# Optimization experiments

Hardware: AMD Instinct MI355X
Metric: run time of the kernel (lower is better)

Reference implementation:

```python
import jax, jax.numpy as jnp
import numpy as np
from jax.scipy.linalg import expm

DIM = 2048        # state dimension (init arg `dim`)
M_STEPS = 8192    # kernel length (init arg `timestamp`)
DELTA = 0.01      # ZOH step size (init arg `delta`)
STAB = 1e-3       # stabilizer added to A before inversion (matches torch code)


def setup_inputs() -> dict:
    key = jax.random.key(0)
    k1, k2, k3 = jax.random.split(key, 3)
    # Match the torch init scaling so matrix_exp/inv stay well-conditioned.
    A = jnp.eye(DIM, dtype=jnp.float32) * -0.01 \
        + jax.random.normal(k1, (DIM, DIM), dtype=jnp.float32) * 0.001
    B = jax.random.normal(k2, (DIM, 1), dtype=jnp.float32) * 0.01
    C = jax.random.normal(k3, (1, DIM), dtype=jnp.float32) * 0.01
    return {"A": A, "B": B, "C": C, "M": M_STEPS}


def reference(A, B, C, M):
    dim = A.shape[0]
    I = jnp.eye(dim, dtype=A.dtype)
    # --- ZOH discretization (torch._zoh_discretize) ---
    A_bar = expm(DELTA * A)                         # [dim, dim]
    A_inv = jnp.linalg.inv(A + STAB * I)            # [dim, dim]
    B_bar = A_inv @ (A_bar - I) @ (DELTA * B)       # [dim, 1]

    # --- kernel power iteration (torch._compute_K_bar) ---
    # K[t] = C @ A_bar^t @ B_bar. Since B_bar is a vector, the serial
    # matrix-power loop reduces to M sequential matvecs (same math).
    def step(x, _):
        term = (C @ x)[0, 0]        # scalar K_t
        return A_bar @ x, term      # advance state: A_bar^{t+1} B_bar

    _, terms = jax.lax.scan(step, B_bar, None, length=M)  # [M]
    K_bar = terms[::-1][None, :]    # flip along time, shape [1, M]
    return K_bar
```

## Files before the change

### kernel.cpp

```cpp
#include <hip/hip_runtime.h>
#include <hip/hip_bf16.h>


#define DIMN 2048
#define MSTEPS 8192
#define RSPLIT 91
#define NSTEPS 90
#define NN ((size_t)DIMN * DIMN)
#define NBLK 32
#define ALD 40
#define GJP 65

typedef short short8 __attribute__((ext_vector_type(8)));
typedef float f32x4 __attribute__((ext_vector_type(4)));

__device__ inline void split1(float x, unsigned short& h, unsigned short& l)
{
  __hip_bfloat16 b = __float2bfloat16(x);
  h = *reinterpret_cast<unsigned short*>(&b);
  float r = x - __bfloat162float(b);
  __hip_bfloat16 b2 = __float2bfloat16(r);
  l = *reinterpret_cast<unsigned short*>(&b2);
}

__global__ __launch_bounds__(256)
void k_combine4(float* out,
                const float* i1, float c1, const float* i2, float c2,
                const float* i3, float c3, const float* i4, float c4,
                float dval)
{
  const int total = DIMN * DIMN;
  for (int idx = blockIdx.x * 256 + threadIdx.x; idx < total; idx += gridDim.x * 256) {
    float v = 0.f;
    if (i1) v = fmaf(c1, i1[idx], v);
    if (i2) v = fmaf(c2, i2[idx], v);
    if (i3) v = fmaf(c3, i3[idx], v);
    if (i4) v = fmaf(c4, i4[idx], v);
    if ((idx >> 11) == (idx & 2047)) v += dval;
    out[idx] = v;
  }
}

__global__ __launch_bounds__(256)
void k_fill64(const float* __restrict__ A, double* __restrict__ M)
{
  const int total = DIMN * DIMN;
  for (int idx = blockIdx.x * 256 + threadIdx.x; idx < total; idx += gridDim.x * 256) {
    double v = (double)A[idx];
    if ((idx >> 11) == (idx & 2047)) v += 1e-3;
    M[idx] = v;
  }
}

__global__ __launch_bounds__(256)
void k_split(const float* __restrict__ in, unsigned short* __restrict__ hi,
             unsigned short* __restrict__ lo)
{
  const int i4 = blockIdx.x * 256 + threadIdx.x;
  const float4 v = ((const float4*)in)[i4];
  ushort4 h, l;
  split1(v.x, h.x, l.x); split1(v.y, h.y, l.y);
  split1(v.z, h.z, l.z); split1(v.w, h.w, l.w);
  ((ushort4*)hi)[i4] = h;
  ((ushort4*)lo)[i4] = l;
}

__global__ __launch_bounds__(256)
void k_splitT(const float* __restrict__ in, unsigned short* __restrict__ hi,
              unsigned short* __restrict__ lo)
{
  __shared__ float t[32][33];
  const int bx = blockIdx.x * 32, by = blockIdx.y * 32;
  const int lx = threadIdx.x, ly = threadIdx.y;
  for (int dy = 0; dy < 32; dy += 8)
    t[ly + dy][lx] = in[(size_t)(by + ly + dy) * DIMN + bx + lx];
  __syncthreads();
  for (int dy = 0; dy < 32; dy += 8) {
    const size_t o = (size_t)(bx + ly + dy) * DIMN + by + lx;
    unsigned short h, l;
    split1(t[lx][ly + dy], h, l);
    hi[o] = h; lo[o] = l;
  }
}

__global__ __launch_bounds__(256)
void k_gemm3(const unsigned short* __restrict__ Ahg, const unsigned short* __restrict__ Alg,
             const unsigned short* __restrict__ Bhg, const unsigned short* __restrict__ Blg,
             float* __restrict__ C, float alpha,
             const float* E1, float c1, const float* E2, float c2)
{
  __shared__ unsigned short sAh[128 * ALD];
  __shared__ unsigned short sAl[128 * ALD];
  __shared__ unsigned short sBh[128 * ALD];
  __shared__ unsigned short sBl[128 * ALD];
  const int tid = threadIdx.x;
  const int wid = tid >> 6, lane = tid & 63;
  const int lr = lane & 15, lg = lane >> 4;
  const int wm = wid >> 1, wn = wid & 1;
  const int brow = blockIdx.y * 128, bcol = blockIdx.x * 128;
  const int sr = tid >> 1, sh = (tid & 1) * 16;

  const unsigned short* gAh = Ahg + (size_t)(brow + sr) * DIMN + sh;
  const unsigned short* gAl = Alg + (size_t)(brow + sr) * DIMN + sh;
  const unsigned short* gBh = Bhg + (size_t)(bcol + sr) * DIMN + sh;
  const unsigned short* gBl = Blg + (size_t)(bcol + sr) * DIMN + sh;

  f32x4 acc[4][4];
#pragma unroll
  for (int mf = 0; mf < 4; ++mf)
#pragma unroll
    for (int nf = 0; nf < 4; ++nf) acc[mf][nf] = (f32x4){0.f, 0.f, 0.f, 0.f};

  uint4 pa0 = *(const uint4*)gAh;      uint4 pa1 = *(const uint4*)(gAh + 8);
  uint4 pb0 = *(const uint4*)gAl;      uint4 pb1 = *(const uint4*)(gAl + 8);
  uint4 pc0 = *(const uint4*)gBh;      uint4 pc1 = *(const uint4*)(gBh + 8);
  uint4 pd0 = *(const uint4*)gBl;      uint4 pd1 = *(const uint4*)(gBl + 8);

  const int nk = DIMN / 32;
  for (int kt = 0; kt < nk; ++kt) {
    *(uint4*)&sAh[sr * ALD + sh] = pa0;  *(uint4*)&sAh[sr * ALD + sh + 8] = pa1;
    *(uint4*)&sAl[sr * ALD + sh] = pb0;  *(uint4*)&sAl[sr * ALD + sh + 8] = pb1;
    *(uint4*)&sBh[sr * ALD + sh] = pc0;  *(uint4*)&sBh[sr * ALD + sh + 8] = pc1;
    *(uint4*)&sBl[sr * ALD + sh] = pd0;  *(uint4*)&sBl[sr * ALD + sh + 8] = pd1;
    __syncthreads();
    if (kt + 1 < nk) {
      const int o = (kt + 1) * 32;
      pa0 = *(const uint4*)(gAh + o);  pa1 = *(const uint4*)(gAh + o + 8);
      pb0 = *(const uint4*)(gAl + o);  pb1 = *(const uint4*)(gAl + o + 8);
      pc0 = *(const uint4*)(gBh + o);  pc1 = *(const uint4*)(gBh + o + 8);
      pd0 = *(const uint4*)(gBl + o);  pd1 = *(const uint4*)(gBl + o + 8);
    }
#pragma unroll
    for (int mf = 0; mf < 4; ++mf) {
      const int ar = 64 * wm + 16 * mf + lr;
      const short8 ah = *(const short8*)&sAh[ar * ALD + lg * 8];
      const short8 al = *(const short8*)&sAl[ar * ALD + lg * 8];
#pragma unroll
      for (int nf = 0; nf < 4; ++nf) {
        const int br = 64 * wn + 16 * nf + lr;
        const short8 bh = *(const short8*)&sBh[br * ALD + lg * 8];
        const short8 bl = *(const short8*)&sBl[br * ALD + lg * 8];
        acc[mf][nf] = __builtin_amdgcn_mfma_f32_16x16x32_bf16(ah, bh, acc[mf][nf], 0, 0, 0);
        acc[mf][nf] = __builtin_amdgcn_mfma_f32_16x16x32_bf16(ah, bl, acc[mf][nf], 0, 0, 0);
        acc[mf][nf] = __builtin_amdgcn_mfma_f32_16x16x32_bf16(al, bh, acc[mf][nf], 0, 0, 0);
      }
    }
    __syncthreads();
  }
#pragma unroll
  for (int mf = 0; mf < 4; ++mf) {
#pragma unroll
    for (int nf = 0; nf < 4; ++nf) {
      const int col = bcol + 64 * wn + 16 * nf + lr;
#pragma unroll
      for (int i = 0; i < 4; ++i) {
        const int row = brow + 64 * wm + 16 * mf + 4 * lg + i;
        float v = alpha * acc[mf][nf][i];
        if (E1) v = fmaf(c1, E1[(size_t)row * DIMN + col], v);
        if (E2) v = fmaf(c2, E2[(size_t)row * DIMN + col], v);
        C[(size_t)row * DIMN + col] = v;
      }
    }
  }
}

#define DBM 64
#define DBK 8
__global__ __launch_bounds__(256)
void k_dgemm(const double* __restrict__ A, int lda,
             const double* __restrict__ B, int ldb,
             double* C, int ldc, int K, double alpha,
             const double* E1, int ld1, double c1)
{
  __shared__ double As[DBK][DBM];
  __shared__ double Bs[DBK][DBM];
  const int tid = threadIdx.x;
  const int tx = tid & 15, ty = tid >> 4;
  const int brow = blockIdx.y * DBM, bcol = blockIdx.x * DBM;

  const int arow = tid >> 2, ac0 = (tid & 3) * 2;
  const int brw  = tid >> 5, bc0 = (tid & 31) * 2;

  const double* Aptr = A + (size_t)(brow + arow) * lda + ac0;
  const double* Bptr = B + (size_t)brw * ldb + (bcol + bc0);

  double2 aPre = *(const double2*)Aptr;
  double2 bPre = *(const double2*)Bptr;

  double acc[4][4];
#pragma unroll
  for (int i = 0; i < 4; ++i)
#pragma unroll
    for (int j = 0; j < 4; ++j) acc[i][j] = 0.0;

  const int nk = K / DBK;
  for (int kt = 0; kt < nk; ++kt) {
    As[ac0 + 0][arow] = aPre.x;
    As[ac0 + 1][arow] = aPre.y;
    Bs[brw][bc0 + 0] = bPre.x;
    Bs[brw][bc0 + 1] = bPre.y;
    __syncthreads();
    if (kt + 1 < nk) {
      aPre = *(const double2*)(Aptr + (size_t)(kt + 1) * DBK);
      bPre = *(const double2*)(Bptr + (size_t)(kt + 1) * DBK * ldb);
    }
#pragma unroll
    for (int kk = 0; kk < DBK; ++kk) {
      double a[4], b[4];
#pragma unroll
      for (int i = 0; i < 4; ++i) a[i] = As[kk][ty * 4 + i];
#pragma unroll
      for (int j = 0; j < 4; ++j) b[j] = Bs[kk][tx * 4 + j];
#pragma unroll
      for (int i = 0; i < 4; ++i)
#pragma unroll
        for (int j = 0; j < 4; ++j)
          acc[i][j] = fma(a[i], b[j], acc[i][j]);
    }
    __syncthreads();
  }
#pragma unroll
  for (int i = 0; i < 4; ++i) {
    const int gi = brow + ty * 4 + i;
#pragma unroll
    for (int j = 0; j < 4; ++j) {
      const int gj = bcol + tx * 4 + j;
      double v = alpha * acc[i][j];
      if (E1) v = fma(c1, E1[(size_t)gi * ld1 + gj], v);
      C[(size_t)gi * ldc + gj] = v;
    }
  }
}

__global__ __launch_bounds__(256)
void k_gj64(const double* __restrict__ M, int ldm, double* __restrict__ W, int ldw)
{
  __shared__ double a[128][GJP];
  const int tid = threadIdx.x;
  const int rg = tid & 7;
  const int cg = tid >> 3;

  for (int idx = tid; idx < 64 * 64; idx += 256) {
    const int r = idx >> 6, c = idx & 63;
    a[c][r] = M[(size_t)r * ldm + c];
    a[64 + c][r] = (r == c) ? 1.0 : 0.0;
  }
  __syncthreads();

  for (int p = 0; p < 64; ++p) {
    const double rpv = 1.0 / a[p][p];
    const int c0 = p + 1 + cg;
    const int c1 = c0 + 32;
    const double prs0 = a[c0][p] * rpv;
    const double prs1 = a[c1][p] * rpv;
    double colp[8];
#pragma unroll
    for (int k = 0; k < 4; ++k) {
      const double2 t2 = *(const double2*)&a[p][rg * 8 + 2 * k];
      colp[2 * k] = t2.x; colp[2 * k + 1] = t2.y;
    }
    __syncthreads();
#pragma unroll
    for (int k = 0; k < 8; ++k) {
      const int r = rg * 8 + k;
      const bool isp = (r == p);
      const double v0 = a[c0][r];
      const double v1 = a[c1][r];
      a[c0][r] = isp ? prs0 : fma(-colp[k], prs0, v0);
      a[c1][r] = isp ? prs1 : fma(-colp[k], prs1, v1);
    }
    __syncthreads();
  }

  for (int idx = tid; idx < 64 * 64; idx += 256) {
    const int r = idx >> 6, c = idx & 63;
    W[(size_t)r * ldw + c] = a[64 + c][r];
  }
}

__global__ __launch_bounds__(256)
void k_stagefix(const double* __restrict__ Dinv, double* __restrict__ M,
                double* __restrict__ Rpan, double* __restrict__ Cpan, int p)
{
  const int blk = blockIdx.x;
  const int tid = threadIdx.x;
  if (blk >= 32) {
    const int idx = (blk - 32) * 256 + tid;
    const int i = idx >> 6, k = idx & 63;
    const bool inP = (i >> 6) == p;
    const size_t mo = (size_t)i * DIMN + p * 64 + k;
    double v = 0.0;
    if (!inP) { v = M[mo]; M[mo] = 0.0; }
    Cpan[idx] = v;
    return;
  }
  __shared__ double As[DBK][DBM];
  __shared__ double Bs[DBK][DBM];
  const double* Mrow = M + (size_t)p * 64 * DIMN;
  const int tx = tid & 15, ty = tid >> 4;
  const int bcol = blk * DBM;

  const int arow = tid >> 2, ac0 = (tid & 3) * 2;
  const int brw  = tid >> 5, bc0 = (tid & 31) * 2;

  const double* Aptr = Dinv + (size_t)arow * 64 + ac0;
  const double* Bptr = Mrow + (size_t)brw * DIMN + (bcol + bc0);

  double2 aPre = *(const double2*)Aptr;
  double2 bPre = *(const double2*)Bptr;

  double acc[4][4];
#pragma unroll
  for (int i = 0; i < 4; ++i)
#pragma unroll
    for (int j = 0; j < 4; ++j) acc[i][j] = 0.0;

  for (int kt = 0; kt < 8; ++kt) {
    As[ac0 + 0][arow] = aPre.x;
    As[ac0 + 1][arow] = aPre.y;
    Bs[brw][bc0 + 0] = bPre.x;
    Bs[brw][bc0 + 1] = bPre.y;
    __syncthreads();
    if (kt + 1 < 8) {
      aPre = *(const double2*)(Aptr + (size_t)(kt + 1) * DBK);
      bPre = *(const double2*)(Bptr + (size_t)(kt + 1) * DBK * DIMN);
    }
#pragma unroll
    for (int kk = 0; kk < DBK; ++kk) {
      double a[4], b[4];
#pragma unroll
      for (int i = 0; i < 4; ++i) a[i] = As[kk][ty * 4 + i];
#pragma unroll
      for (int j = 0; j < 4; ++j) b[j] = Bs[kk][tx * 4 + j];
#pragma unroll
      for (int i = 0; i < 4; ++i)
#pragma unroll
        for (int j = 0; j < 4; ++j)
          acc[i][j] = fma(a[i], b[j], acc[i][j]);
    }
    __syncthreads();
  }
  const bool pivcol = (bcol >> 6) == p;
#pragma unroll
  for (int i = 0; i < 4; ++i) {
    const int gi = ty * 4 + i;
#pragma unroll
    for (int j = 0; j < 4; ++j) {
      const int gj = bcol + tx * 4 + j;
      double v = pivcol ? Dinv[(size_t)gi * 64 + (gj & 63)] : acc[i][j];
      Rpan[(size_t)gi * DIMN + gj] = v;
      M[(size_t)(p * 64 + gi) * DIMN + gj] = v;
    }
  }
}

__global__ __launch_bounds__(256)
void k_mv(const float* __restrict__ Mat, const double* __restrict__ vin,
          double* vout, const double* vadd, double alpha)
{
  const int lane = threadIdx.x & 63;
  const int row = blockIdx.x * 4 + (threadIdx.x >> 6);
  const float* mrow = Mat + (size_t)row * DIMN;
  double acc = 0.0;
  for (int p = 0; p < DIMN; p += 256) {
    const float4 m = *(const float4*)&mrow[p + lane * 4];
    const double* vp = &vin[p + lane * 4];
    acc += (double)m.x * vp[0] + (double)m.y * vp[1] + (double)m.z * vp[2] + (double)m.w * vp[3];
  }
  for (int off = 32; off; off >>= 1) acc += __shfl_down(acc, off);
  if (lane == 0) vout[row] = alpha * acc + (vadd ? vadd[row] : 0.0);
}

__global__ __launch_bounds__(256)
void k_mv64(const double* __restrict__ W, const double* __restrict__ vin,
            double* vout, const double* vadd, double alpha)
{
  const int lane = threadIdx.x & 63;
  const int row = blockIdx.x * 4 + (threadIdx.x >> 6);
  const double* mrow = W + (size_t)row * DIMN;
  double acc = 0.0;
  for (int p = 0; p < DIMN; p += 256) {
    const int idx = p + lane * 4;
    const double2 m0 = *(const double2*)&mrow[idx];
    const double2 m1 = *(const double2*)&mrow[idx + 2];
    acc += m0.x * vin[idx] + m0.y * vin[idx + 1] + m1.x * vin[idx + 2] + m1.y * vin[idx + 3];
  }
  for (int off = 32; off; off >>= 1) acc += __shfl_down(acc, off);
  if (lane == 0) vout[row] = alpha * acc + (vadd ? vadd[row] : 0.0);
}

__global__ __launch_bounds__(256)
void k_mvres(const float* __restrict__ A, const double* __restrict__ x,
             const double* __restrict__ y, double* r)
{
  const int lane = threadIdx.x & 63;
  const int row = blockIdx.x * 4 + (threadIdx.x >> 6);
  const float* mrow = A + (size_t)row * DIMN;
  double acc = 0.0;
  for (int p = 0; p < DIMN; p += 256) {
    const float4 m = *(const float4*)&mrow[p + lane * 4];
    const double* vp = &x[p + lane * 4];
    acc += (double)m.x * vp[0] + (double)m.y * vp[1] + (double)m.z * vp[2] + (double)m.w * vp[3];
  }
  for (int off = 32; off; off >>= 1) acc += __shfl_down(acc, off);
  if (lane == 0) r[row] = y[row] - acc - 1e-3 * x[row];
}

__global__ __launch_bounds__(256)
void k_transpose(const float* __restrict__ in, float* __restrict__ out)
{
  __shared__ float t[32][33];
  const int bx = blockIdx.x * 32, by = blockIdx.y * 32;
  const int lx = threadIdx.x, ly = threadIdx.y;
  for (int dy = 0; dy < 32; dy += 8)
    t[ly + dy][lx] = in[(size_t)(by + ly + dy) * DIMN + bx + lx];
  __syncthreads();
  for (int dy = 0; dy < 32; dy += 8)
    out[(size_t)(bx + ly + dy) * DIMN + by + lx] = t[lx][ly + dy];
}

__global__ __launch_bounds__(256)
void k_chain(const float* __restrict__ E, const float* __restrict__ vin, float* __restrict__ vout,
             const float* __restrict__ ERT, const float* __restrict__ uin, float* __restrict__ uout)
{
  const int lane = threadIdx.x & 63;
  const int w = threadIdx.x >> 6;
  const int b = blockIdx.x;
  const float* mrow; const float* xin; float* xout; int row;
  if (b < 512) { row = b * 4 + w; mrow = E + (size_t)row * DIMN; xin = vin; xout = vout; }
  else { row = (b - 512) * 4 + w; mrow = ERT + (size_t)row * DIMN; xin = uin; xout = uout; }
  float acc = 0.f;
  for (int p = 0; p < DIMN; p += 256) {
    const float4 m = *(const float4*)&mrow[p + lane * 4];
    const float* vp = &xin[p + lane * 4];
    acc = fmaf(m.x, vp[0], acc);
    acc = fmaf(m.y, vp[1], acc);
    acc = fmaf(m.z, vp[2], acc);
    acc = fmaf(m.w, vp[3], acc);
  }
  for (int off = 32; off; off >>= 1) acc += __shfl_down(acc, off);
  if (lane == 0) xout[row] = xin[row] + acc;
}

__global__ __launch_bounds__(256)
void k_terms(const float* __restrict__ U, const float* __restrict__ V, float* __restrict__ out)
{
  const int lane = threadIdx.x & 63;
  const int t = blockIdx.x * 4 + (threadIdx.x >> 6);
  const int j = t / RSPLIT, i = t - j * RSPLIT;
  const float* u = U + (size_t)j * DIMN;
  const float* v = V + (size_t)i * DIMN;
  float acc = 0.f;
  for (int p = 0; p < DIMN; p += 256) {
    const float4 a4 = *(const float4*)&u[p + lane * 4];
    const float4 b4 = *(const float4*)&v[p + lane * 4];
    acc = fmaf(a4.x, b4.x, acc); acc = fmaf(a4.y, b4.y, acc);
    acc = fmaf(a4.z, b4.z, acc); acc = fmaf(a4.w, b4.w, acc);
  }
  for (int off = 32; off; off >>= 1) acc += __shfl_down(acc, off);
  if (lane == 0) out[MSTEPS - 1 - t] = acc;
}

__global__ void k_vecinit(const float* __restrict__ B, double* __restrict__ b64,
                          const float* __restrict__ Cv, float* __restrict__ U0)
{
  const int i = blockIdx.x * 256 + threadIdx.x;
  if (i < DIMN) { b64[i] = 0.01 * (double)B[i]; U0[i] = Cv[i]; }
}
__global__ void k_v0(const double* __restrict__ x64, float* __restrict__ V0)
{
  const int i = blockIdx.x * 256 + threadIdx.x;
  if (i < DIMN) V0[i] = (float)x64[i];
}

extern "C" void kernel_launch(void* const* d_in, const int* in_sizes, int n_in,
                              void* d_out, int out_size, void* d_ws, size_t ws_size,
                              hipStream_t stream)
{
  const float* dA = (const float*)d_in[0];
  const float* dB = (const float*)d_in[1];
  const float* dC = (const float*)d_in[2];
  float* out = (float*)d_out;

  float* fb = (float*)d_ws;
  float* Ebuf = fb;
  float* t1 = fb + NN;
  float* t2 = t1 + NN;
  float* t3 = t2 + NN;
  float* t4 = t3 + NN;
  double* M64 = (double*)t1;
  double* scr64 = (double*)(fb + 5 * NN);
  double* Dinv = scr64;
  double* Cpan = Dinv + 64 * 64;
  double* Rpan = Cpan + (size_t)DIMN * 64;
  double* y64 = Rpan + (size_t)DIMN * 64;
  double* x64 = y64 + DIMN;
  double* r64 = x64 + DIMN;
  double* b64 = r64 + DIMN;
  float* V  = (float*)(b64 + DIMN);
  float* Uc = V + (size_t)RSPLIT * DIMN;

  const size_t needed = 5 * NN * 4
                        + (64 * 64 + 2 * (size_t)DIMN * 64 + 4 * (size_t)DIMN) * 8
                        + (size_t)(2 * RSPLIT) * DIMN * 4;
  if (ws_size < needed) return;

  const float* NUL = nullptr;
  dim3 cb(256), cg(2048);

  unsigned short* Ah  = (unsigned short*)t4;   unsigned short* Al  = Ah + NN;
  unsigned short* Ath = (unsigned short*)Ebuf; unsigned short* Atl = Ath + NN;
  unsigned short* Y2h = (unsigned short*)t1;   unsigned short* Y2l = Y2h + NN;
  unsigned short* Hth = (unsigned short*)t2;   unsigned short* Htl = Hth + NN;

  k_split<<<dim3(4096), cb, 0, stream>>>(dA, Ah, Al);
  k_splitT<<<dim3(64, 64), dim3(32, 8), 0, stream>>>(dA, Ath, Atl);
  k_gemm3<<<dim3(16, 16), cb, 0, stream>>>(Ah, Al, Ath, Atl, t3, 0.8281f,
                                           NUL, 0.f, NUL, 0.f);
  k_combine4<<<cg, cb, 0, stream>>>(Ebuf, t3, (float)(5e-5 / 0.8281), dA, 0.01f,
                                    NUL, 0, NUL, 0, 0.f);

  k_fill64<<<cg, cb, 0, stream>>>(dA, M64);
  for (int p = 0; p < NBLK; ++p) {
    double* Mrow = M64 + (size_t)p * 64 * DIMN;
    k_gj64<<<dim3(1), cb, 0, stream>>>(Mrow + p * 64, DIMN, Dinv, 64);
    k_stagefix<<<dim3(544), cb, 0, stream>>>(Dinv, M64, Rpan, Cpan, p);
    k_dgemm<<<dim3(32, 32), cb, 0, stream>>>(Cpan, 64, Rpan, DIMN, M64, DIMN, 64, -1.0,
                                             M64, DIMN, 1.0);
  }

  k_vecinit<<<dim3(8), cb, 0, stream>>>(dB, b64, dC, Uc);
  k_mv<<<dim3(512), cb, 0, stream>>>(Ebuf, b64, y64, (const double*)nullptr, 1.0);
  k_mv64<<<dim3(512), cb, 0, stream>>>(M64, y64, x64, (const double*)nullptr, 1.0);
  k_mvres<<<dim3(512), cb, 0, stream>>>(dA, x64, y64, r64);
  k_mv64<<<dim3(512), cb, 0, stream>>>(M64, r64, x64, x64, 1.0);
  k_v0<<<dim3(8), cb, 0, stream>>>(x64, V);

  k_combine4<<<cg, cb, 0, stream>>>(t4, dA, 0.91f / 6.f, t3, 1.f / 24.f,
                                    NUL, 0, NUL, 0, 0.f);
  k_split<<<dim3(4096), cb, 0, stream>>>(t3, Y2h, Y2l);
  k_splitT<<<dim3(64, 64), dim3(32, 8), 0, stream>>>(t4, Hth, Htl);
  k_gemm3<<<dim3(16, 16), cb, 0, stream>>>(Y2h, Y2l, Hth, Htl, t3, 1.f,
                                           t3, 0.5f, dA, 0.91f);
  k_transpose<<<dim3(64, 64), dim3(32, 8), 0, stream>>>(t3, t4);

  for (int s = 0; s < NSTEPS; ++s) {
    k_chain<<<dim3(1024), cb, 0, stream>>>(Ebuf, V + (size_t)s * DIMN, V + (size_t)(s + 1) * DIMN,
                                           t4, Uc + (size_t)s * DIMN, Uc + (size_t)(s + 1) * DIMN);
  }
  k_terms<<<dim3(2048), cb, 0, stream>>>(Uc, V, out);
}
```

Before: 4.190 ms.

## Batch chain matvecs using higher matrix powers to cut serial launches

```diff
diff --git a/kernel.cpp b/kernel.cpp
--- a/kernel.cpp
+++ b/kernel.cpp
@@ -5,10 +5,9 @@
 #define DIMN 2048
 #define MSTEPS 8192
 #define RSPLIT 91
-#define NSTEPS 90
 #define NN ((size_t)DIMN * DIMN)
 #define NBLK 32
-#define ALD 40
+#define ALD 36
 #define GJP 65
 
 typedef short short8 __attribute__((ext_vector_type(8)));
@@ -130,6 +129,13 @@
       pc0 = *(const uint4*)(gBh + o);  pc1 = *(const uint4*)(gBh + o + 8);
       pd0 = *(const uint4*)(gBl + o);  pd1 = *(const uint4*)(gBl + o + 8);
     }
+    short8 bh[4], bl[4];
+#pragma unroll
+    for (int nf = 0; nf < 4; ++nf) {
+      const int br = 64 * wn + 16 * nf + lr;
+      bh[nf] = *(const short8*)&sBh[br * ALD + lg * 8];
+      bl[nf] = *(const short8*)&sBl[br * ALD + lg * 8];
+    }
 #pragma unroll
     for (int mf = 0; mf < 4; ++mf) {
       const int ar = 64 * wm + 16 * mf + lr;
@@ -137,12 +143,9 @@
       const short8 al = *(const short8*)&sAl[ar * ALD + lg * 8];
 #pragma unroll
       for (int nf = 0; nf < 4; ++nf) {
-        const int br = 64 * wn + 16 * nf + lr;
-        const short8 bh = *(const short8*)&sBh[br * ALD + lg * 8];
-        const short8 bl = *(const short8*)&sBl[br * ALD + lg * 8];
-        acc[mf][nf] = __builtin_amdgcn_mfma_f32_16x16x32_bf16(ah, bh, acc[mf][nf], 0, 0, 0);
-        acc[mf][nf] = __builtin_amdgcn_mfma_f32_16x16x32_bf16(ah, bl, acc[mf][nf], 0, 0, 0);
-        acc[mf][nf] = __builtin_amdgcn_mfma_f32_16x16x32_bf16(al, bh, acc[mf][nf], 0, 0, 0);
+        acc[mf][nf] = __builtin_amdgcn_mfma_f32_16x16x32_bf16(ah, bh[nf], acc[mf][nf], 0, 0, 0);
+        acc[mf][nf] = __builtin_amdgcn_mfma_f32_16x16x32_bf16(ah, bl[nf], acc[mf][nf], 0, 0, 0);
+        acc[mf][nf] = __builtin_amdgcn_mfma_f32_16x16x32_bf16(al, bh[nf], acc[mf][nf], 0, 0, 0);
       }
     }
     __syncthreads();
@@ -443,6 +446,65 @@
 }
 
 __global__ __launch_bounds__(256)
+void k_chainb(const float* __restrict__ E8, const float* __restrict__ Vin,
+              float* __restrict__ Vout, int do_v,
+              const float* __restrict__ A4T, const float* __restrict__ Uin,
+              float* __restrict__ Uout)
+{
+  const int lane = threadIdx.x & 63;
+  const int w = threadIdx.x >> 6;
+  const int b = blockIdx.x;
+  if (b < 512) {
+    if (!do_v) return;
+    const int row = b * 4 + w;
+    const float* mrow = E8 + (size_t)row * DIMN;
+    float acc[8];
+#pragma unroll
+    for (int r = 0; r < 8; ++r) acc[r] = 0.f;
+    for (int p = 0; p < DIMN; p += 256) {
+      const float4 m = *(const float4*)&mrow[p + lane * 4];
+#pragma unroll
+      for (int r = 0; r < 8; ++r) {
+        const float4 v = *(const float4*)&Vin[(size_t)r * DIMN + p + lane * 4];
+        acc[r] = fmaf(m.x, v.x, acc[r]);
+        acc[r] = fmaf(m.y, v.y, acc[r]);
+        acc[r] = fmaf(m.z, v.z, acc[r]);
+        acc[r] = fmaf(m.w, v.w, acc[r]);
+      }
+    }
+#pragma unroll
+    for (int r = 0; r < 8; ++r) {
+      float a = acc[r];
+      for (int off = 32; off; off >>= 1) a += __shfl_down(a, off);
+      if (lane == 0) Vout[(size_t)r * DIMN + row] = Vin[(size_t)r * DIMN + row] + a;
+    }
+  } else {
+    const int row = (b - 512) * 4 + w;
+    const float* mrow = A4T + (size_t)row * DIMN;
+    float acc[4];
+#pragma unroll
+    for (int r = 0; r < 4; ++r) acc[r] = 0.f;
+    for (int p = 0; p < DIMN; p += 256) {
+      const float4 m = *(const float4*)&mrow[p + lane * 4];
+#pragma unroll
+      for (int r = 0; r < 4; ++r) {
+        const float4 v = *(const float4*)&Uin[(size_t)r * DIMN + p + lane * 4];
+        acc[r] = fmaf(m.x, v.x, acc[r]);
+        acc[r] = fmaf(m.y, v.y, acc[r]);
+        acc[r] = fmaf(m.z, v.z, acc[r]);
+        acc[r] = fmaf(m.w, v.w, acc[r]);
+      }
+    }
+#pragma unroll
+    for (int r = 0; r < 4; ++r) {
+      float a = acc[r];
+      for (int off = 32; off; off >>= 1) a += __shfl_down(a, off);
+      if (lane == 0) Uout[(size_t)r * DIMN + row] = Uin[(size_t)r * DIMN + row] + a;
+    }
+  }
+}
+
+__global__ __launch_bounds__(256)
 void k_terms(const float* __restrict__ U, const float* __restrict__ V, float* __restrict__ out)
 {
   const int lane = threadIdx.x & 63;
@@ -488,8 +550,9 @@
   float* t2 = t1 + NN;
   float* t3 = t2 + NN;
   float* t4 = t3 + NN;
+  float* t5 = t4 + NN;
   double* M64 = (double*)t1;
-  double* scr64 = (double*)(fb + 5 * NN);
+  double* scr64 = (double*)(fb + 6 * NN);
   double* Dinv = scr64;
   double* Cpan = Dinv + 64 * 64;
   double* Rpan = Cpan + (size_t)DIMN * 64;
@@ -498,11 +561,11 @@
   double* r64 = x64 + DIMN;
   double* b64 = r64 + DIMN;
   float* V  = (float*)(b64 + DIMN);
-  float* Uc = V + (size_t)RSPLIT * DIMN;
-
-  const size_t needed = 5 * NN * 4
+  float* Uc = V + (size_t)96 * DIMN;
+
+  const size_t needed = 6 * NN * 4
                         + (64 * 64 + 2 * (size_t)DIMN * 64 + 4 * (size_t)DIMN) * 8
-                        + (size_t)(2 * RSPLIT) * DIMN * 4;
+                        + (size_t)(96 + 92) * DIMN * 4;
   if (ws_size < needed) return;
 
   const float* NUL = nullptr;
@@ -540,13 +603,26 @@
                                     NUL, 0, NUL, 0, 0.f);
   k_split<<<dim3(4096), cb, 0, stream>>>(t3, Y2h, Y2l);
   k_splitT<<<dim3(64, 64), dim3(32, 8), 0, stream>>>(t4, Hth, Htl);
-  k_gemm3<<<dim3(16, 16), cb, 0, stream>>>(Y2h, Y2l, Hth, Htl, t3, 1.f,
+  k_gemm3<<<dim3(16, 16), cb, 0, stream>>>(Y2h, Y2l, Hth, Htl, t4, 1.f,
                                            t3, 0.5f, dA, 0.91f);
-  k_transpose<<<dim3(64, 64), dim3(32, 8), 0, stream>>>(t3, t4);
-
-  for (int s = 0; s < NSTEPS; ++s) {
+  k_transpose<<<dim3(64, 64), dim3(32, 8), 0, stream>>>(t4, t5);
+  k_combine4<<<cg, cb, 0, stream>>>(t4, dA, 3.64f / 6.f, t3, 16.f / 24.f,
+                                    NUL, 0, NUL, 0, 0.f);
+  k_splitT<<<dim3(64, 64), dim3(32, 8), 0, stream>>>(t4, Hth, Htl);
+  k_gemm3<<<dim3(16, 16), cb, 0, stream>>>(Y2h, Y2l, Hth, Htl, t4, 16.f,
+                                           t3, 8.f, dA, 3.64f);
+  k_combine4<<<cg, cb, 0, stream>>>(t1, dA, 0.08f, t3, (float)(0.0032 / 0.8281),
+                                    NUL, 0, NUL, 0, 0.f);
+  k_transpose<<<dim3(64, 64), dim3(32, 8), 0, stream>>>(t4, t3);
+
+  for (int s = 0; s < 7; ++s) {
     k_chain<<<dim3(1024), cb, 0, stream>>>(Ebuf, V + (size_t)s * DIMN, V + (size_t)(s + 1) * DIMN,
-                                           t4, Uc + (size_t)s * DIMN, Uc + (size_t)(s + 1) * DIMN);
+                                           t5, Uc + (size_t)s * DIMN, Uc + (size_t)(s + 1) * DIMN);
+  }
+  for (int i = 0; i < 22; ++i) {
+    k_chainb<<<dim3(1024), cb, 0, stream>>>(
+        t1, V + (size_t)(8 * i) * DIMN, V + (size_t)(8 * i + 8) * DIMN, (i < 11) ? 1 : 0,
+        t3, Uc + (size_t)(4 * i) * DIMN, Uc + (size_t)(4 * i + 4) * DIMN);
   }
   k_terms<<<dim3(2048), cb, 0, stream>>>(Uc, V, out);
 }
```

Result: no change. 4.229 ms (+0.9%).
